# Optimization experiments

Measured on AMD Instinct MI355X. Metric: run time of the kernel, lower is better.

The kernel has to match this reference:

```python
import jax, jax.numpy as jnp
import numpy as np

jax.config.update("jax_enable_x64", True)  # exact int64 fixed-point requantization

QMIN, QMAX = 0, 255  # 8-bit asymmetric activations


def _mul_m0_shift(acc, M0, shift):
    """gemmlowp-style fixed-point rescale: round((acc*M0)>>31) >> shift (rounding)."""
    prod = acc.astype(jnp.int64) * M0.astype(jnp.int64)
    nudge = jnp.where(prod >= 0, jnp.int64(1 << 30), jnp.int64(1 - (1 << 30)))
    hi = (prod + nudge) >> 31  # rounding-doubling high mul
    sh = shift.astype(jnp.int64)
    return (hi + (jnp.int64(1) << (sh - 1))) >> sh  # rounding right shift


def _requant(acc, M0, shift, z_out):
    return jnp.clip(_mul_m0_shift(acc, M0, shift) + z_out, QMIN, QMAX).astype(jnp.int32)


def _qconv(q, w, z_in, M0, shift, z_out, pad):
    # int8-style conv: subtract input zero-point, integer accumulate (exact in fp32
    # since |acc| < 2^24 by construction), then fixed-point requantize.
    xf = (q - z_in).astype(jnp.float32)
    acc = jax.lax.conv_general_dilated(
        xf, w, (1, 1), [(pad, pad), (pad, pad)],
        dimension_numbers=("NCHW", "OIHW", "NCHW"))
    return _requant(jnp.round(acc).astype(jnp.int64), M0, shift, z_out)


def _qbn(q, z_in, w, b, M0, shift, z_out):
    # fused quantized BN: per-channel integer affine + fixed-point requantize
    acc = (q.astype(jnp.int64) - z_in) * w.astype(jnp.int64)[None, :, None, None] \
          + b.astype(jnp.int64)[None, :, None, None]
    return _requant(acc, M0, shift, z_out)


def setup_inputs() -> dict:
    key = jax.random.key(0)
    ks = jax.random.split(key, 10)
    B, Cin, H, W = 32, 256, 56, 56
    width, Cout = 64, 256
    x = jax.random.randint(ks[0], (B, Cin, H, W), 0, 256, dtype=jnp.int32)
    w1 = jax.random.randint(ks[1], (width, Cin, 1, 1), -63, 64).astype(jnp.float32)
    w2 = jax.random.randint(ks[2], (width, width, 3, 3), -63, 64).astype(jnp.float32)
    w3 = jax.random.randint(ks[3], (Cout, width, 1, 1), -63, 64).astype(jnp.float32)
    bn1_w = jax.random.randint(ks[4], (width,), 100, 160).astype(jnp.float32)
    bn1_b = jax.random.randint(ks[5], (width,), -1000, 1000).astype(jnp.float32)
    bn2_w = jax.random.randint(ks[6], (width,), 100, 160).astype(jnp.float32)
    bn2_b = jax.random.randint(ks[7], (width,), -1000, 1000).astype(jnp.float32)
    bn3_w = jax.random.randint(ks[8], (Cout,), 100, 160).astype(jnp.float32)
    bn3_b = jax.random.randint(ks[9], (Cout,), -1000, 1000).astype(jnp.float32)
    conv_zin = jnp.array([128, 128, 128], jnp.int32)
    conv_m0 = jnp.array([1518500250] * 3, jnp.int32)
    conv_shift = jnp.array([9, 9, 9], jnp.int32)
    conv_zout = jnp.array([128, 128, 128], jnp.int32)
    bn_m0 = jnp.array([1073741824] * 3, jnp.int32)
    bn_shift = jnp.array([6, 6, 6], jnp.int32)
    bn_zout = jnp.array([128, 128, 128], jnp.int32)
    add_z = jnp.array([128, 128], jnp.int32)
    add_m0 = jnp.array([1073741824] * 2, jnp.int32)
    add_shift = jnp.array([1, 1], jnp.int32)
    add_zout = jnp.array(128, jnp.int32)
    return dict(x=x, w1=w1, w2=w2, w3=w3,
                bn1_w=bn1_w, bn1_b=bn1_b, bn2_w=bn2_w, bn2_b=bn2_b,
                bn3_w=bn3_w, bn3_b=bn3_b,
                conv_zin=conv_zin, conv_m0=conv_m0, conv_shift=conv_shift,
                conv_zout=conv_zout, bn_m0=bn_m0, bn_shift=bn_shift,
                bn_zout=bn_zout, add_z=add_z, add_m0=add_m0,
                add_shift=add_shift, add_zout=add_zout)


def reference(x, w1, w2, w3, bn1_w, bn1_b, bn2_w, bn2_b, bn3_w, bn3_b,
              conv_zin, conv_m0, conv_shift, conv_zout,
              bn_m0, bn_shift, bn_zout,
              add_z, add_m0, add_shift, add_zout):
    identity = x  # a_bit == target_bit -> rescale_matrix path skipped, conv_x = x
    out = _qconv(x, w1, conv_zin[0], conv_m0[0], conv_shift[0], conv_zout[0], 0)
    out = _qbn(out, conv_zout[0], bn1_w, bn1_b, bn_m0[0], bn_shift[0], bn_zout[0])
    out = _qconv(out, w2, conv_zin[1], conv_m0[1], conv_shift[1], conv_zout[1], 1)
    out = _qbn(out, conv_zout[1], bn2_w, bn2_b, bn_m0[1], bn_shift[1], bn_zout[1])
    out = _qconv(out, w3, conv_zin[2], conv_m0[2], conv_shift[2], conv_zout[2], 0)
    out = _qbn(out, conv_zout[2], bn3_w, bn3_b, bn_m0[2], bn_shift[2], bn_zout[2])
    # QuantizedAdd: rescale both branches to the output scale, add, clamp
    ra = _mul_m0_shift(identity.astype(jnp.int64) - add_z[0], add_m0[0], add_shift[0])
    rb = _mul_m0_shift(out.astype(jnp.int64) - add_z[1], add_m0[1], add_shift[1])
    return jnp.clip(ra + rb + add_zout, QMIN, QMAX).astype(jnp.int32)
```

## Files before the change

kernel.cpp:

```cpp
#include <hip/hip_runtime.h>


typedef int v4i __attribute__((ext_vector_type(4)));

#define BATCH 32
#define CIN 256
#define CMID 64
#define HW 3136
#define W56 56
#define WP_BYTES ((size_t)68 * 64 * 16)

__device__ __forceinline__ int requant_f(int acc, int M0, long long pAdd,
                                         long long nAdd, int tSh, int zout) {
    long long prod = (long long)acc * (long long)M0;
    long long add = (prod >= 0) ? pAdd : nAdd;
    int v = (int)((prod + add) >> tSh) + zout;
    return v < 0 ? 0 : (v > 255 ? 255 : v);
}

__device__ __forceinline__ v4i pack16f(const float* src, int stride) {
    v4i r;
#pragma unroll
    for (int d = 0; d < 4; ++d) {
        unsigned int u = 0;
#pragma unroll
        for (int by = 0; by < 4; ++by) {
            int v = (int)src[(d * 4 + by) * stride];
            u |= ((unsigned int)(v & 255)) << (8 * by);
        }
        r[d] = (int)u;
    }
    return r;
}

__global__ __launch_bounds__(256) void k_prep(
    const float* __restrict__ w1, const float* __restrict__ w2,
    const float* __restrict__ w3, v4i* __restrict__ wp)
{
    int id = blockIdx.x * 256 + threadIdx.x;
    int fid = id >> 6, lane = id & 63;
    if (fid >= 68) return;
    int col = lane & 15, ci0 = (lane >> 4) * 16;
    const float* src;
    int stride;
    if (fid < 16) {
        int wv = fid >> 2, ks = fid & 3;
        src = w1 + (size_t)(wv * 16 + col) * 256 + ks * 64 + ci0;
        stride = 1;
    } else if (fid < 52) {
        int i = fid - 16, wv = i / 9, t = i - wv * 9;
        src = w2 + ((size_t)(wv * 16 + col) * 64 + ci0) * 9 + t;
        stride = 9;
    } else {
        int s = fid - 52;
        src = w3 + (size_t)(s * 16 + col) * 64 + ci0;
        stride = 1;
    }
    wp[fid * 64 + lane] = pack16f(src, stride);
}

__global__ __launch_bounds__(256, 2) void k_fused(
    const int* __restrict__ x, const v4i* __restrict__ wp,
    const float* __restrict__ bn1_w, const float* __restrict__ bn1_b,
    const float* __restrict__ bn2_w, const float* __restrict__ bn2_b,
    const float* __restrict__ bn3_w, const float* __restrict__ bn3_b,
    const int* __restrict__ conv_zin, const int* __restrict__ conv_m0,
    const int* __restrict__ conv_shift, const int* __restrict__ conv_zout,
    const int* __restrict__ bn_m0, const int* __restrict__ bn_shift,
    const int* __restrict__ bn_zout,
    const int* __restrict__ add_z, const int* __restrict__ add_m0,
    const int* __restrict__ add_shift, const int* __restrict__ add_zout,
    int* __restrict__ out)
{
    __shared__ v4i smX[1680];
    __shared__ v4i smM[1740];
    __shared__ int lutA[256], lutB[256];

    const int tid = threadIdx.x, lane = tid & 63, wv = tid >> 6;
    const int col = lane & 15, koff = lane >> 4;
    const int b = blockIdx.y, r0 = blockIdx.x * 4;
    const int rowb = koff * 4;
    const int co0 = wv * 16;

    {
        const int az0 = add_z[0], az1 = add_z[1];
        const int am0 = add_m0[0], am1 = add_m0[1];
        const int ash0 = add_shift[0], ash1 = add_shift[1];
        const int azout = add_zout[0];
        long long pA = (long long)(tid - az0) * am0;
        long long pB = (long long)(tid - az1) * am1;
        long long P0 = (1LL << 30) + (1LL << (30 + ash0));
        long long N0 = (1LL - (1LL << 30)) + (1LL << (30 + ash0));
        long long P1 = (1LL << 30) + (1LL << (30 + ash1));
        long long N1 = (1LL - (1LL << 30)) + (1LL << (30 + ash1));
        lutA[tid] = (int)((pA + (pA >= 0 ? P0 : N0)) >> (31 + ash0));
        lutB[tid] = (int)((pB + (pB >= 0 ? P1 : N1)) >> (31 + ash1)) + azout;
    }
    if (tid < 192) {
        int e = tid >> 4, d = tid & 15;
        int row = e >> 1, side = e & 1;
        ((int*)smM)[(row * 58 + side * 57) * 20 + d] = 0;
    }

    const int zin = conv_zin[0];
    v4i a1[4];
#pragma unroll
    for (int ks = 0; ks < 4; ++ks) a1[ks] = wp[(wv * 4 + ks) * 64 + lane];

    v4i accA[21];
#pragma unroll
    for (int i = 0; i < 21; ++i) accA[i] = (v4i){0, 0, 0, 0};

    unsigned long long* smuX = (unsigned long long*)smX;
    for (int ks = 0; ks < 4; ++ks) {
        if (ks) __syncthreads();
#pragma unroll
        for (int u = 0; u < 3; ++u) {
            int unit = tid + u * 256;
            if (unit < 672) {
                int cg = unit & 7, qq = unit >> 3;
                int row = qq / 14, quad = qq - row * 14;
                int grow = r0 - 1 + row;
                v4i xa[8];
                if ((unsigned)grow < 56u) {
                    const int* xb = x + (size_t)(b * CIN + ks * 64 + cg * 8) * HW
                                      + grow * W56 + quad * 4;
#pragma unroll
                    for (int j = 0; j < 8; ++j)
                        xa[j] = *(const v4i*)(xb + (size_t)j * HW);
                } else {
#pragma unroll
                    for (int j = 0; j < 8; ++j) {
                        v4i z; z[0] = zin; z[1] = zin; z[2] = zin; z[3] = zin;
                        xa[j] = z;
                    }
                }
#pragma unroll
                for (int p = 0; p < 4; ++p) {
                    unsigned int lo = 0, hi = 0;
#pragma unroll
                    for (int j = 0; j < 4; ++j) {
                        lo |= ((unsigned int)((xa[j][p] - zin) & 255)) << (8 * j);
                        hi |= ((unsigned int)((xa[j + 4][p] - zin) & 255)) << (8 * j);
                    }
                    smuX[(qq * 4 + p) * 10 + cg] = ((unsigned long long)hi << 32) | lo;
                }
            }
        }
        __syncthreads();
#pragma unroll
        for (int nt = 0; nt < 21; ++nt) {
            v4i bf = smX[(nt * 16 + col) * 5 + koff];
            accA[nt] = __builtin_amdgcn_mfma_i32_16x16x64_i8(a1[ks], bf, accA[nt], 0, 0, 0);
        }
    }

    {
        const int cm0 = conv_m0[0], csh = conv_shift[0], czo = conv_zout[0];
        const int bm0 = bn_m0[0], bsh = bn_shift[0], bzo = bn_zout[0];
        const long long cP = (1LL << 30) + (1LL << (30 + csh));
        const long long cN = (1LL - (1LL << 30)) + (1LL << (30 + csh));
        const long long bP = (1LL << 30) + (1LL << (30 + bsh));
        const long long bN = (1LL - (1LL << 30)) + (1LL << (30 + bsh));
        const int cT = 31 + csh, bT = 31 + bsh;
        const int zin2 = conv_zin[1];
        int bw[4], bb[4];
#pragma unroll
        for (int r = 0; r < 4; ++r) {
            bw[r] = (int)bn1_w[co0 + rowb + r];
            bb[r] = (int)bn1_b[co0 + rowb + r];
        }
#pragma unroll
        for (int nt = 0; nt < 21; ++nt) {
            int px = nt * 16 + col;
            int row = px / W56, gw = px - row * W56;
            int grow = r0 - 1 + row;
            unsigned int pkd = 0;
            if ((unsigned)grow < 56u) {
#pragma unroll
                for (int r = 0; r < 4; ++r) {
                    int q1 = requant_f(accA[nt][r], cm0, cP, cN, cT, czo);
                    int a2 = (q1 - czo) * bw[r] + bb[r];
                    int q2 = requant_f(a2, bm0, bP, bN, bT, bzo);
                    pkd |= ((unsigned int)((q2 - zin2) & 255)) << (8 * r);
                }
            }
            ((int*)smM)[(row * 58 + 1 + gw) * 20 + wv * 4 + koff] = (int)pkd;
        }
    }
    __syncthreads();

    v4i a2f[9];
#pragma unroll
    for (int t = 0; t < 9; ++t) a2f[t] = wp[(16 + wv * 9 + t) * 64 + lane];

    int basep[14];
#pragma unroll
    for (int nt = 0; nt < 14; ++nt) {
        int pix = nt * 16 + col;
        int orow = pix / W56, wc = pix - orow * W56;
        basep[nt] = (orow * 58 + wc) * 5 + koff;
    }

    v4i accB[14];
#pragma unroll
    for (int i = 0; i < 14; ++i) accB[i] = (v4i){0, 0, 0, 0};
#pragma unroll
    for (int kh = 0; kh < 3; ++kh) {
#pragma unroll
        for (int kw = 0; kw < 3; ++kw) {
            v4i af = a2f[kh * 3 + kw];
            const int toff = (kh * 58 + kw) * 5;
#pragma unroll
            for (int nt = 0; nt < 14; ++nt) {
                v4i bf = smM[basep[nt] + toff];
                accB[nt] = __builtin_amdgcn_mfma_i32_16x16x64_i8(af, bf, accB[nt], 0, 0, 0);
            }
        }
    }

    {
        const int cm0 = conv_m0[1], csh = conv_shift[1], czo = conv_zout[1];
        const int bm0 = bn_m0[1], bsh = bn_shift[1], bzo = bn_zout[1];
        const long long cP = (1LL << 30) + (1LL << (30 + csh));
        const long long cN = (1LL - (1LL << 30)) + (1LL << (30 + csh));
        const long long bP = (1LL << 30) + (1LL << (30 + bsh));
        const long long bN = (1LL - (1LL << 30)) + (1LL << (30 + bsh));
        const int cT = 31 + csh, bT = 31 + bsh;
        const int zin3 = conv_zin[2];
        int bw[4], bb[4];
#pragma unroll
        for (int r = 0; r < 4; ++r) {
            bw[r] = (int)bn2_w[co0 + rowb + r];
            bb[r] = (int)bn2_b[co0 + rowb + r];
        }
#pragma unroll
        for (int nt = 0; nt < 14; ++nt) {
            unsigned int pkd = 0;
#pragma unroll
            for (int r = 0; r < 4; ++r) {
                int q1 = requant_f(accB[nt][r], cm0, cP, cN, cT, czo);
                int a2 = (q1 - czo) * bw[r] + bb[r];
                int q2 = requant_f(a2, bm0, bP, bN, bT, bzo);
                pkd |= ((unsigned int)((q2 - zin3) & 255)) << (8 * r);
            }
            ((int*)smX)[(nt * 16 + col) * 20 + wv * 4 + koff] = (int)pkd;
        }
    }

    v4i a3f[4];
#pragma unroll
    for (int f = 0; f < 4; ++f) a3f[f] = wp[(52 + wv * 4 + f) * 64 + lane];
    const int ghw0 = r0 * W56;
    int xcur[4][4], xnxt[4][4];
#pragma unroll
    for (int f = 0; f < 4; ++f)
#pragma unroll
        for (int r = 0; r < 4; ++r)
            xcur[f][r] = x[(size_t)(b * CIN + wv * 64 + f * 16 + rowb + r) * HW + ghw0 + col];
    __syncthreads();

    {
        const int cm0 = conv_m0[2], csh = conv_shift[2], czo = conv_zout[2];
        const int bm0 = bn_m0[2], bsh = bn_shift[2], bzo = bn_zout[2];
        const long long cP = (1LL << 30) + (1LL << (30 + csh));
        const long long cN = (1LL - (1LL << 30)) + (1LL << (30 + csh));
        const long long bP = (1LL << 30) + (1LL << (30 + bsh));
        const long long bN = (1LL - (1LL << 30)) + (1LL << (30 + bsh));
        const int cT = 31 + csh, bT = 31 + bsh;
        int bw[4][4], bb[4][4];
#pragma unroll
        for (int f = 0; f < 4; ++f)
#pragma unroll
            for (int r = 0; r < 4; ++r) {
                bw[f][r] = (int)bn3_w[wv * 64 + f * 16 + rowb + r];
                bb[f][r] = (int)bn3_b[wv * 64 + f * 16 + rowb + r];
            }
        const v4i zf = (v4i){0, 0, 0, 0};
#pragma unroll
        for (int nt = 0; nt < 14; ++nt) {
            if (nt < 13) {
#pragma unroll
                for (int f = 0; f < 4; ++f)
#pragma unroll
                    for (int r = 0; r < 4; ++r)
                        xnxt[f][r] = x[(size_t)(b * CIN + wv * 64 + f * 16 + rowb + r) * HW
                                       + ghw0 + (nt + 1) * 16 + col];
            }
            v4i bf = smX[(nt * 16 + col) * 5 + koff];
            v4i accC[4];
#pragma unroll
            for (int f = 0; f < 4; ++f)
                accC[f] = __builtin_amdgcn_mfma_i32_16x16x64_i8(a3f[f], bf, zf, 0, 0, 0);
#pragma unroll
            for (int f = 0; f < 4; ++f)
#pragma unroll
                for (int r = 0; r < 4; ++r) {
                    int q1 = requant_f(accC[f][r], cm0, cP, cN, cT, czo);
                    int a2 = (q1 - czo) * bw[f][r] + bb[f][r];
                    int q2 = requant_f(a2, bm0, bP, bN, bT, bzo);
                    int res = lutA[xcur[f][r]] + lutB[q2];
                    res = res < 0 ? 0 : (res > 255 ? 255 : res);
                    out[(size_t)(b * CIN + wv * 64 + f * 16 + rowb + r) * HW
                        + ghw0 + nt * 16 + col] = res;
                }
#pragma unroll
            for (int f = 0; f < 4; ++f)
#pragma unroll
                for (int r = 0; r < 4; ++r) xcur[f][r] = xnxt[f][r];
        }
    }
}

extern "C" void kernel_launch(void* const* d_in, const int* in_sizes, int n_in,
                              void* d_out, int out_size, void* d_ws, size_t ws_size,
                              hipStream_t stream) {
    const int* x = (const int*)d_in[0];
    const float* w1 = (const float*)d_in[1];
    const float* w2 = (const float*)d_in[2];
    const float* w3 = (const float*)d_in[3];
    const float* bn1_w = (const float*)d_in[4];
    const float* bn1_b = (const float*)d_in[5];
    const float* bn2_w = (const float*)d_in[6];
    const float* bn2_b = (const float*)d_in[7];
    const float* bn3_w = (const float*)d_in[8];
    const float* bn3_b = (const float*)d_in[9];
    const int* conv_zin = (const int*)d_in[10];
    const int* conv_m0 = (const int*)d_in[11];
    const int* conv_shift = (const int*)d_in[12];
    const int* conv_zout = (const int*)d_in[13];
    const int* bn_m0 = (const int*)d_in[14];
    const int* bn_shift = (const int*)d_in[15];
    const int* bn_zout = (const int*)d_in[16];
    const int* add_z = (const int*)d_in[17];
    const int* add_m0 = (const int*)d_in[18];
    const int* add_shift = (const int*)d_in[19];
    const int* add_zout = (const int*)d_in[20];

    v4i* wp = (v4i*)d_ws;

    k_prep<<<dim3(17), dim3(256), 0, stream>>>(w1, w2, w3, wp);
    k_fused<<<dim3(14, 32), dim3(256), 0, stream>>>(x, wp,
        bn1_w, bn1_b, bn2_w, bn2_b, bn3_w, bn3_b,
        conv_zin, conv_m0, conv_shift, conv_zout, bn_m0, bn_shift, bn_zout,
        add_z, add_m0, add_shift, add_zout, (int*)d_out);
}
```

Baseline: 281.5 us.

## Halve row tile, raise occupancy, fold input zero-point into row-sum correction

```diff
diff --git a/kernel.cpp b/kernel.cpp
--- a/kernel.cpp
+++ b/kernel.cpp
@@ -5,7 +5,6 @@
 
 #define BATCH 32
 #define CIN 256
-#define CMID 64
 #define HW 3136
 #define W56 56
 #define WP_BYTES ((size_t)68 * 64 * 16)
@@ -18,6 +17,17 @@
     return v < 0 ? 0 : (v > 255 ? 255 : v);
 }
 
+__device__ __forceinline__ unsigned pk4(unsigned x0, unsigned x1,
+                                        unsigned x2, unsigned x3) {
+#if __has_builtin(__builtin_amdgcn_perm)
+    unsigned t01 = __builtin_amdgcn_perm(x1, x0, 0x0400u);
+    unsigned t23 = __builtin_amdgcn_perm(x3, x2, 0x0400u);
+    return __builtin_amdgcn_perm(t23, t01, 0x05040100u);
+#else
+    return (x0 & 255u) | ((x1 & 255u) << 8) | ((x2 & 255u) << 16) | (x3 << 24);
+#endif
+}
+
 __device__ __forceinline__ v4i pack16f(const float* src, int stride) {
     v4i r;
 #pragma unroll
@@ -35,32 +45,39 @@
 
 __global__ __launch_bounds__(256) void k_prep(
     const float* __restrict__ w1, const float* __restrict__ w2,
-    const float* __restrict__ w3, v4i* __restrict__ wp)
+    const float* __restrict__ w3, v4i* __restrict__ wp, int* __restrict__ rs)
 {
     int id = blockIdx.x * 256 + threadIdx.x;
     int fid = id >> 6, lane = id & 63;
-    if (fid >= 68) return;
-    int col = lane & 15, ci0 = (lane >> 4) * 16;
-    const float* src;
-    int stride;
-    if (fid < 16) {
-        int wv = fid >> 2, ks = fid & 3;
-        src = w1 + (size_t)(wv * 16 + col) * 256 + ks * 64 + ci0;
-        stride = 1;
-    } else if (fid < 52) {
-        int i = fid - 16, wv = i / 9, t = i - wv * 9;
-        src = w2 + ((size_t)(wv * 16 + col) * 64 + ci0) * 9 + t;
-        stride = 9;
-    } else {
-        int s = fid - 52;
-        src = w3 + (size_t)(s * 16 + col) * 64 + ci0;
-        stride = 1;
-    }
-    wp[fid * 64 + lane] = pack16f(src, stride);
-}
-
-__global__ __launch_bounds__(256, 2) void k_fused(
+    if (fid < 68) {
+        int col = lane & 15, ci0 = (lane >> 4) * 16;
+        const float* src;
+        int stride;
+        if (fid < 16) {
+            int wv = fid >> 2, ks = fid & 3;
+            src = w1 + (size_t)(wv * 16 + col) * 256 + ks * 64 + ci0;
+            stride = 1;
+        } else if (fid < 52) {
+            int i = fid - 16, wv = i / 9, t = i - wv * 9;
+            src = w2 + ((size_t)(wv * 16 + col) * 64 + ci0) * 9 + t;
+            stride = 9;
+        } else {
+            int s = fid - 52;
+            src = w3 + (size_t)(s * 16 + col) * 64 + ci0;
+            stride = 1;
+        }
+        wp[fid * 64 + lane] = pack16f(src, stride);
+    }
+    if (id < 64) {
+        int s = 0;
+        for (int ci = 0; ci < 256; ++ci) s += (int)w1[id * 256 + ci];
+        rs[id] = s;
+    }
+}
+
+__global__ __launch_bounds__(256, 4) void k_fused(
     const int* __restrict__ x, const v4i* __restrict__ wp,
+    const int* __restrict__ rs,
     const float* __restrict__ bn1_w, const float* __restrict__ bn1_b,
     const float* __restrict__ bn2_w, const float* __restrict__ bn2_b,
     const float* __restrict__ bn3_w, const float* __restrict__ bn3_b,
@@ -72,13 +89,15 @@
     const int* __restrict__ add_shift, const int* __restrict__ add_zout,
     int* __restrict__ out)
 {
-    __shared__ v4i smX[1680];
-    __shared__ v4i smM[1740];
+    __shared__ v4i smX[1120];
+    __shared__ v4i smM[1160];
     __shared__ int lutA[256], lutB[256];
 
     const int tid = threadIdx.x, lane = tid & 63, wv = tid >> 6;
     const int col = lane & 15, koff = lane >> 4;
-    const int b = blockIdx.y, r0 = blockIdx.x * 4;
+    const int lin = blockIdx.y * 28 + blockIdx.x;
+    const int wrk = (lin & 7) * 112 + (lin >> 3);
+    const int b = wrk / 28, r0 = (wrk - b * 28) * 2;
     const int rowb = koff * 4;
     const int co0 = wv * 16;
 
@@ -96,7 +115,7 @@
         lutA[tid] = (int)((pA + (pA >= 0 ? P0 : N0)) >> (31 + ash0));
         lutB[tid] = (int)((pB + (pB >= 0 ? P1 : N1)) >> (31 + ash1)) + azout;
     }
-    if (tid < 192) {
+    if (tid < 128) {
         int e = tid >> 4, d = tid & 15;
         int row = e >> 1, side = e & 1;
         ((int*)smM)[(row * 58 + side * 57) * 20 + d] = 0;
@@ -107,49 +126,47 @@
 #pragma unroll
     for (int ks = 0; ks < 4; ++ks) a1[ks] = wp[(wv * 4 + ks) * 64 + lane];
 
-    v4i accA[21];
-#pragma unroll
-    for (int i = 0; i < 21; ++i) accA[i] = (v4i){0, 0, 0, 0};
+    v4i accA[14];
+#pragma unroll
+    for (int i = 0; i < 14; ++i) accA[i] = (v4i){0, 0, 0, 0};
 
     unsigned long long* smuX = (unsigned long long*)smX;
+#pragma unroll
     for (int ks = 0; ks < 4; ++ks) {
         if (ks) __syncthreads();
 #pragma unroll
-        for (int u = 0; u < 3; ++u) {
+        for (int u = 0; u < 2; ++u) {
             int unit = tid + u * 256;
-            if (unit < 672) {
+            if (unit < 448) {
                 int cg = unit & 7, qq = unit >> 3;
                 int row = qq / 14, quad = qq - row * 14;
                 int grow = r0 - 1 + row;
-                v4i xa[8];
                 if ((unsigned)grow < 56u) {
                     const int* xb = x + (size_t)(b * CIN + ks * 64 + cg * 8) * HW
                                       + grow * W56 + quad * 4;
+                    v4i xa[8];
 #pragma unroll
                     for (int j = 0; j < 8; ++j)
                         xa[j] = *(const v4i*)(xb + (size_t)j * HW);
+#pragma unroll
+                    for (int p = 0; p < 4; ++p) {
+                        unsigned lo = pk4(xa[0][p], xa[1][p], xa[2][p], xa[3][p])
+                                      ^ 0x80808080u;
+                        unsigned hi = pk4(xa[4][p], xa[5][p], xa[6][p], xa[7][p])
+                                      ^ 0x80808080u;
+                        smuX[(qq * 4 + p) * 10 + cg] =
+                            ((unsigned long long)hi << 32) | lo;
+                    }
                 } else {
 #pragma unroll
-                    for (int j = 0; j < 8; ++j) {
-                        v4i z; z[0] = zin; z[1] = zin; z[2] = zin; z[3] = zin;
-                        xa[j] = z;
-                    }
+                    for (int p = 0; p < 4; ++p)
+                        smuX[(qq * 4 + p) * 10 + cg] = 0ull;
                 }
-#pragma unroll
-                for (int p = 0; p < 4; ++p) {
-                    unsigned int lo = 0, hi = 0;
-#pragma unroll
-                    for (int j = 0; j < 4; ++j) {
-                        lo |= ((unsigned int)((xa[j][p] - zin) & 255)) << (8 * j);
-                        hi |= ((unsigned int)((xa[j + 4][p] - zin) & 255)) << (8 * j);
-                    }
-                    smuX[(qq * 4 + p) * 10 + cg] = ((unsigned long long)hi << 32) | lo;
-                }
             }
         }
         __syncthreads();
 #pragma unroll
-        for (int nt = 0; nt < 21; ++nt) {
+        for (int nt = 0; nt < 14; ++nt) {
             v4i bf = smX[(nt * 16 + col) * 5 + koff];
             accA[nt] = __builtin_amdgcn_mfma_i32_16x16x64_i8(a1[ks], bf, accA[nt], 0, 0, 0);
         }
@@ -164,14 +181,15 @@
         const long long bN = (1LL - (1LL << 30)) + (1LL << (30 + bsh));
         const int cT = 31 + csh, bT = 31 + bsh;
         const int zin2 = conv_zin[1];
-        int bw[4], bb[4];
+        int bw[4], bb[4], corr[4];
 #pragma unroll
         for (int r = 0; r < 4; ++r) {
             bw[r] = (int)bn1_w[co0 + rowb + r];
             bb[r] = (int)bn1_b[co0 + rowb + r];
-        }
-#pragma unroll
-        for (int nt = 0; nt < 21; ++nt) {
+            corr[r] = (128 - zin) * rs[co0 + rowb + r];
+        }
+#pragma unroll
+        for (int nt = 0; nt < 14; ++nt) {
             int px = nt * 16 + col;
             int row = px / W56, gw = px - row * W56;
             int grow = r0 - 1 + row;
@@ -179,7 +197,7 @@
             if ((unsigned)grow < 56u) {
 #pragma unroll
                 for (int r = 0; r < 4; ++r) {
-                    int q1 = requant_f(accA[nt][r], cm0, cP, cN, cT, czo);
+                    int q1 = requant_f(accA[nt][r] + corr[r], cm0, cP, cN, cT, czo);
                     int a2 = (q1 - czo) * bw[r] + bb[r];
                     int q2 = requant_f(a2, bm0, bP, bN, bT, bzo);
                     pkd |= ((unsigned int)((q2 - zin2) & 255)) << (8 * r);
@@ -194,17 +212,17 @@
 #pragma unroll
     for (int t = 0; t < 9; ++t) a2f[t] = wp[(16 + wv * 9 + t) * 64 + lane];
 
-    int basep[14];
-#pragma unroll
-    for (int nt = 0; nt < 14; ++nt) {
+    int basep[7];
+#pragma unroll
+    for (int nt = 0; nt < 7; ++nt) {
         int pix = nt * 16 + col;
         int orow = pix / W56, wc = pix - orow * W56;
         basep[nt] = (orow * 58 + wc) * 5 + koff;
     }
 
-    v4i accB[14];
-#pragma unroll
-    for (int i = 0; i < 14; ++i) accB[i] = (v4i){0, 0, 0, 0};
+    v4i accB[7];
+#pragma unroll
+    for (int i = 0; i < 7; ++i) accB[i] = (v4i){0, 0, 0, 0};
 #pragma unroll
     for (int kh = 0; kh < 3; ++kh) {
 #pragma unroll
@@ -212,7 +230,7 @@
             v4i af = a2f[kh * 3 + kw];
             const int toff = (kh * 58 + kw) * 5;
 #pragma unroll
-            for (int nt = 0; nt < 14; ++nt) {
+            for (int nt = 0; nt < 7; ++nt) {
                 v4i bf = smM[basep[nt] + toff];
                 accB[nt] = __builtin_amdgcn_mfma_i32_16x16x64_i8(af, bf, accB[nt], 0, 0, 0);
             }
@@ -235,7 +253,7 @@
             bb[r] = (int)bn2_b[co0 + rowb + r];
         }
 #pragma unroll
-        for (int nt = 0; nt < 14; ++nt) {
+        for (int nt = 0; nt < 7; ++nt) {
             unsigned int pkd = 0;
 #pragma unroll
             for (int r = 0; r < 4; ++r) {
@@ -257,7 +275,8 @@
     for (int f = 0; f < 4; ++f)
 #pragma unroll
         for (int r = 0; r < 4; ++r)
-            xcur[f][r] = x[(size_t)(b * CIN + wv * 64 + f * 16 + rowb + r) * HW + ghw0 + col];
+            xcur[f][r] = x[(size_t)(b * CIN + wv * 64 + f * 16 + rowb + r) * HW
+                           + ghw0 + col];
     __syncthreads();
 
     {
@@ -278,8 +297,8 @@
             }
         const v4i zf = (v4i){0, 0, 0, 0};
 #pragma unroll
-        for (int nt = 0; nt < 14; ++nt) {
-            if (nt < 13) {
+        for (int nt = 0; nt < 7; ++nt) {
+            if (nt < 6) {
 #pragma unroll
                 for (int f = 0; f < 4; ++f)
 #pragma unroll
@@ -338,9 +357,10 @@
     const int* add_zout = (const int*)d_in[20];
 
     v4i* wp = (v4i*)d_ws;
-
-    k_prep<<<dim3(17), dim3(256), 0, stream>>>(w1, w2, w3, wp);
-    k_fused<<<dim3(14, 32), dim3(256), 0, stream>>>(x, wp,
+    int* rs = (int*)((char*)d_ws + WP_BYTES);
+
+    k_prep<<<dim3(17), dim3(256), 0, stream>>>(w1, w2, w3, wp, rs);
+    k_fused<<<dim3(28, 32), dim3(256), 0, stream>>>(x, wp, rs,
         bn1_w, bn1_b, bn2_w, bn2_b, bn3_w, bn3_b,
         conv_zin, conv_m0, conv_shift, conv_zout, bn_m0, bn_shift, bn_zout,
         add_z, add_m0, add_shift, add_zout, (int*)d_out);
```

Result: slower. 409.4 us (+45.4%).
